# Optimization experiments

Measured on AMD Instinct MI355X. Metric: run time of the kernel, lower is better.

The kernel has to match this reference:

```python
import jax, jax.numpy as jnp
import numpy as np

INPUT_DIM = 2
COUNT_BINS = 16
BOUND = 5.0
FLOW_LENGTH = 4
HIDDEN = 256
MULT = 4 * COUNT_BINS - 1  # 63 param groups per dim (w:K, h:K, d:K-1, lam:K)
MIN_BIN = 1e-3
MIN_DERIV = 1e-3
MIN_LAMBDA = 0.025
N = 131072


def _masks():
    input_idx = np.arange(1, INPUT_DIM + 1)                  # [2]
    hidden_idx = np.arange(HIDDEN) % (INPUT_DIM - 1) + 1     # all ones for input_dim=2
    out_idx = np.tile(input_idx, MULT)                       # [126] -> [1,2,1,2,...]
    m1 = (hidden_idx[:, None] >= input_idx[None, :]).astype(np.float32)   # [H,2]
    m2 = (hidden_idx[:, None] >= hidden_idx[None, :]).astype(np.float32)  # [H,H]
    m3 = (out_idx[:, None] > hidden_idx[None, :]).astype(np.float32)      # [126,H]
    return jnp.asarray(m1), jnp.asarray(m2), jnp.asarray(m3)


def _made(z, W1, b1, W2, b2, W3, b3, m1, m2, m3):
    # masked MLP producing raw spline params, shape [..., MULT, input_dim]
    h = jax.nn.relu(z @ (W1 * m1).T + b1)
    h = jax.nn.relu(h @ (W2 * m2).T + b2)
    out = (h @ (W3 * m3).T + b3).reshape(z.shape[:-1] + (MULT, INPUT_DIM))
    K = COUNT_BINS
    sw = lambda t: jnp.swapaxes(t, -1, -2)  # -> [..., input_dim, K]
    w = sw(out[..., 0:K, :])
    hh = sw(out[..., K:2 * K, :])
    d = sw(out[..., 2 * K:3 * K - 1, :])
    lam = sw(out[..., 3 * K - 1:4 * K - 1, :])
    return w, hh, d, lam


def _spline(x, w_raw, h_raw, d_raw, l_raw):
    # Pyro monotonic linear rational spline (Dolatabadi et al.), forward only.
    K = COUNT_BINS
    left, right = -BOUND, BOUND
    w = jax.nn.softmax(w_raw, axis=-1)
    h = jax.nn.softmax(h_raw, axis=-1)
    d = jax.nn.softplus(d_raw)
    l = jax.nn.sigmoid(l_raw)

    widths = MIN_BIN + (1.0 - MIN_BIN * K) * w
    zpad = jnp.zeros(widths.shape[:-1] + (1,), widths.dtype)
    cw = jnp.concatenate([zpad, jnp.cumsum(widths, -1)], -1)
    cw = (right - left) * cw + left
    cw = cw.at[..., 0].set(left).at[..., -1].set(right)
    widths = cw[..., 1:] - cw[..., :-1]

    heights = MIN_BIN + (1.0 - MIN_BIN * K) * h
    ch = jnp.concatenate([zpad, jnp.cumsum(heights, -1)], -1)
    ch = (right - left) * ch + left
    ch = ch.at[..., 0].set(left).at[..., -1].set(right)
    heights = ch[..., 1:] - ch[..., :-1]

    deriv = MIN_DERIV + d
    onep = jnp.ones(deriv.shape[:-1] + (1,), deriv.dtype)
    deriv = jnp.concatenate([onep, deriv, onep], -1)  # boundary derivs = 1, [.., K+1]

    lam = MIN_LAMBDA + (1.0 - 2.0 * MIN_LAMBDA) * l

    inside = (x >= left) & (x <= right)
    xc = jnp.clip(x, left, right)

    bin_idx = jnp.clip(jnp.sum((xc[..., None] >= cw).astype(jnp.int32), -1) - 1, 0, K - 1)
    ib = bin_idx[..., None]
    g = lambda t: jnp.take_along_axis(t, ib, -1)[..., 0]
    x_k = g(cw)
    w_k = g(widths)
    y_k = g(ch)
    h_k = g(heights)
    d_k = g(deriv)
    d_k1 = jnp.take_along_axis(deriv, ib + 1, -1)[..., 0]
    lam_k = g(lam)

    wa = 1.0
    wb = jnp.sqrt(d_k / d_k1) * wa
    wc = (lam_k * wa * d_k + (1.0 - lam_k) * wb * d_k1) * (w_k / h_k)
    ya = y_k
    yb = h_k + y_k
    yc = ((1.0 - lam_k) * wa * ya + lam_k * wb * yb) / ((1.0 - lam_k) * wa + lam_k * wb)

    theta = (xc - x_k) / w_k
    left_seg = theta <= lam_k
    num = jnp.where(left_seg,
                    wa * ya * (lam_k - theta) + wc * yc * theta,
                    wc * yc * (1.0 - theta) + wb * yb * (theta - lam_k))
    den = jnp.where(left_seg,
                    wa * (lam_k - theta) + wc * theta,
                    wc * (1.0 - theta) + wb * (theta - lam_k))
    y = num / den
    return jnp.where(inside, y, x)  # identity outside [-B, B]


def setup_inputs() -> dict:
    key = jax.random.key(0)
    ks = jax.random.split(key, 7)
    s = 0.05
    return {
        "x": jax.random.normal(ks[0], (N, INPUT_DIM), jnp.float32),
        "W1": jax.random.normal(ks[1], (HIDDEN, INPUT_DIM), jnp.float32) * s,
        "b1": jax.random.normal(ks[2], (HIDDEN,), jnp.float32) * s,
        "W2": jax.random.normal(ks[3], (HIDDEN, HIDDEN), jnp.float32) * s,
        "b2": jax.random.normal(ks[4], (HIDDEN,), jnp.float32) * s,
        "W3": jax.random.normal(ks[5], (MULT * INPUT_DIM, HIDDEN), jnp.float32) * s,
        "b3": jax.random.normal(ks[6], (MULT * INPUT_DIM,), jnp.float32) * s,
    }


def reference(x, W1, b1, W2, b2, W3, b3):
    # forward(): apply the SAME shared spline transform flow_length times,
    # collecting intermediates zs (returned stacked: [L+1, N, 2]).
    m1, m2, m3 = _masks()
    z = x
    zs = [z]
    for _ in range(FLOW_LENGTH):
        w, hh, d, l = _made(z, W1, b1, W2, b2, W3, b3, m1, m2, m3)
        z = _spline(z, w, hh, d, l)
        zs.append(z)
    return jnp.stack(zs)
```

## Files before the change

kernel.cpp:

```cpp
#include <hip/hip_runtime.h>
#include <hip/hip_fp16.h>
#include <math.h>

#define N_SAMPLES 131072
#define HIDDEN    256
#define M_GRID    2048
#define REC       72
#define U_LO      (-8.0f)
#define DELTA     0.0078125f
#define INV_DELTA 128.0f
#define MT3       16
#define STR2      69

__device__ __attribute__((aligned(16))) float g_H2T[M_GRID * HIDDEN];
__device__ __attribute__((aligned(16))) float g_table[M_GRID * REC];
__device__ __attribute__((aligned(16))) float g_knots0[REC];

__device__ __forceinline__ float rcpf(float x) { return __builtin_amdgcn_rcpf(x); }

__device__ __forceinline__ float softplusf(float x) {
  return fmaxf(x, 0.0f) + log1pf(expf(-fabsf(x)));
}

__device__ __forceinline__ unsigned int packh2(float a, float b) {
  __half2 h = __floats2half2_rn(a, b);
  return *(unsigned int*)&h;
}

__device__ __forceinline__ void unpack8(uint4 u, float* f) {
  float2 t;
  t = __half22float2(*(__half2*)&u.x); f[0] = t.x; f[1] = t.y;
  t = __half22float2(*(__half2*)&u.y); f[2] = t.x; f[3] = t.y;
  t = __half22float2(*(__half2*)&u.z); f[4] = t.x; f[5] = t.y;
  t = __half22float2(*(__half2*)&u.w); f[6] = t.x; f[7] = t.y;
}

__device__ void process_column(const float* __restrict__ raw, int stride,
                               float* __restrict__ rec) {
  float v[16];
  float cw[17], ch[17], dv[17], lm[16];
  float mx = -1e30f;
#pragma unroll
  for (int k = 0; k < 16; k++) { v[k] = raw[k * stride]; mx = fmaxf(mx, v[k]); }
  float s = 0.0f;
#pragma unroll
  for (int k = 0; k < 16; k++) { v[k] = expf(v[k] - mx); s += v[k]; }
  float scl = 0.984f / s;
  cw[0] = -5.0f;
  float a = 0.0f;
#pragma unroll
  for (int k = 0; k < 16; k++) {
    a += fmaf(v[k], scl, 0.001f);
    cw[k + 1] = fmaf(a, 10.0f, -5.0f);
  }
  cw[16] = 5.0f;
  mx = -1e30f;
#pragma unroll
  for (int k = 0; k < 16; k++) { v[k] = raw[(16 + k) * stride]; mx = fmaxf(mx, v[k]); }
  s = 0.0f;
#pragma unroll
  for (int k = 0; k < 16; k++) { v[k] = expf(v[k] - mx); s += v[k]; }
  scl = 0.984f / s;
  ch[0] = -5.0f;
  a = 0.0f;
#pragma unroll
  for (int k = 0; k < 16; k++) {
    a += fmaf(v[k], scl, 0.001f);
    ch[k + 1] = fmaf(a, 10.0f, -5.0f);
  }
  ch[16] = 5.0f;
  dv[0] = 1.0f; dv[16] = 1.0f;
#pragma unroll
  for (int j = 0; j < 15; j++) dv[j + 1] = 0.001f + softplusf(raw[(32 + j) * stride]);
#pragma unroll
  for (int k = 0; k < 16; k++) {
    float xx = raw[(47 + k) * stride];
    lm[k] = fmaf(0.95f, 1.0f / (1.0f + expf(-xx)), 0.025f);
  }
  uint4* u4 = (uint4*)rec;
  u4[0] = make_uint4(packh2(cw[0], cw[1]),  packh2(cw[2], cw[3]),
                     packh2(cw[4], cw[5]),  packh2(cw[6], cw[7]));
  u4[1] = make_uint4(packh2(cw[8], cw[9]),  packh2(cw[10], cw[11]),
                     packh2(cw[12], cw[13]), packh2(cw[14], cw[15]));
#pragma unroll
  for (int k = 0; k < 16; k++) {
    u4[2 + k] = make_uint4(packh2(ch[k], ch[k + 1]), packh2(dv[k], dv[k + 1]),
                           packh2(lm[k], cw[k]),     packh2(cw[k + 1], 0.0f));
  }
}

__device__ __forceinline__ float spline_eval(float z, float xk, float xk1,
                                             float yk, float yk1,
                                             float dk, float dk1, float lam) {
  float xc = fminf(fmaxf(z, -5.0f), 5.0f);
  float wk = xk1 - xk;
  float hk = yk1 - yk;
  float wb = __builtin_amdgcn_sqrtf(dk * rcpf(dk1));
  float wc = fmaf(lam, dk, (1.0f - lam) * wb * dk1) * wk * rcpf(hk);
  float ya = yk;
  float yb = yk + hk;
  float yc = fmaf(lam * wb, yb, (1.0f - lam) * ya) * rcpf(fmaf(lam, wb, 1.0f - lam));
  float th = (xc - xk) * rcpf(wk);
  bool left = th <= lam;
  float num = left ? fmaf(ya, lam - th, wc * yc * th)
                   : fmaf(wc * yc, 1.0f - th, wb * yb * (th - lam));
  float den = left ? fmaf(wc, th, lam - th)
                   : fmaf(wc, 1.0f - th, wb * (th - lam));
  float y = num * rcpf(den);
  bool inside = (z >= -5.0f) && (z <= 5.0f);
  return inside ? y : z;
}

__global__ __launch_bounds__(256) void k_gemm2(const float* __restrict__ W1,
                                               const float* __restrict__ b1,
                                               const float* __restrict__ W2,
                                               const float* __restrict__ b2) {
  __shared__ unsigned int sW[128 * STR2];
  __shared__ float2 sAB[256];
  __shared__ float red[3 * 64 * 36];
  const int t = threadIdx.x;
  const int m0 = blockIdx.x * 32;
  const int o0 = blockIdx.y * 64;
  {
    const int ol = t >> 2, seg = t & 3;
    const float* src = W2 + (size_t)(o0 + ol) * 256 + 16 * seg;
#pragma unroll
    for (int c = 0; c < 4; c++) {
#pragma unroll
      for (int q = 0; q < 4; q++) {
        float4 v = *(const float4*)(src + 64 * c + 4 * q);
        const int k2 = (64 * c + 16 * seg + 4 * q) >> 1;
        sW[(k2 + 0) * STR2 + ol] = packh2(v.x, v.y);
        sW[(k2 + 1) * STR2 + ol] = packh2(v.z, v.w);
      }
    }
  }
  sAB[t] = make_float2(W1[2 * t], b1[t]);
  __syncthreads();
  const int w = t >> 6, lane = t & 63;
  const int tp = lane >> 2, tm = lane & 3;
  const float u0 = fmaf((float)(m0 + 8 * tm), DELTA, U_LO);
  float acc[4][8] = {};
  const int kb2 = w * 32;
#pragma unroll 4
  for (int kk = 0; kk < 32; kk++) {
    const int k2 = kb2 + kk;
    uint4 ap = *(const uint4*)&sW[k2 * STR2 + 4 * tp];
    float2 a0 = __half22float2(*(__half2*)&ap.x);
    float2 a1 = __half22float2(*(__half2*)&ap.y);
    float2 a2 = __half22float2(*(__half2*)&ap.z);
    float2 a3 = __half22float2(*(__half2*)&ap.w);
    float2 abe = sAB[2 * k2];
    float2 abo = sAB[2 * k2 + 1];
    float t0e = fmaf(abe.x, u0, abe.y), ste = abe.x * DELTA;
    float t0o = fmaf(abo.x, u0, abo.y), sto = abo.x * DELTA;
    float he[8], ho[8];
#pragma unroll
    for (int j = 0; j < 8; j++) {
      he[j] = fmaxf(fmaf((float)j, ste, t0e), 0.0f);
      ho[j] = fmaxf(fmaf((float)j, sto, t0o), 0.0f);
    }
#pragma unroll
    for (int j = 0; j < 8; j++) {
      acc[0][j] = fmaf(a0.x, he[j], acc[0][j]);
      acc[1][j] = fmaf(a1.x, he[j], acc[1][j]);
      acc[2][j] = fmaf(a2.x, he[j], acc[2][j]);
      acc[3][j] = fmaf(a3.x, he[j], acc[3][j]);
      acc[0][j] = fmaf(a0.y, ho[j], acc[0][j]);
      acc[1][j] = fmaf(a1.y, ho[j], acc[1][j]);
      acc[2][j] = fmaf(a2.y, ho[j], acc[2][j]);
      acc[3][j] = fmaf(a3.y, ho[j], acc[3][j]);
    }
  }
  if (w > 0) {
#pragma unroll
    for (int i = 0; i < 4; i++) {
      *(float4*)&red[((w - 1) * 64 + lane) * 36 + 8 * i] =
          make_float4(acc[i][0], acc[i][1], acc[i][2], acc[i][3]);
      *(float4*)&red[((w - 1) * 64 + lane) * 36 + 8 * i + 4] =
          make_float4(acc[i][4], acc[i][5], acc[i][6], acc[i][7]);
    }
  }
  __syncthreads();
  if (w == 0) {
#pragma unroll
    for (int v = 0; v < 3; v++) {
#pragma unroll
      for (int i = 0; i < 4; i++) {
        float4 r0 = *(const float4*)&red[(v * 64 + lane) * 36 + 8 * i];
        float4 r1 = *(const float4*)&red[(v * 64 + lane) * 36 + 8 * i + 4];
        acc[i][0] += r0.x; acc[i][1] += r0.y; acc[i][2] += r0.z; acc[i][3] += r0.w;
        acc[i][4] += r1.x; acc[i][5] += r1.y; acc[i][6] += r1.z; acc[i][7] += r1.w;
      }
    }
    float4 bb = *(const float4*)&b2[o0 + 4 * tp];
#pragma unroll
    for (int j = 0; j < 8; j++) {
      float4 r;
      r.x = fmaxf(acc[0][j] + bb.x, 0.0f);
      r.y = fmaxf(acc[1][j] + bb.y, 0.0f);
      r.z = fmaxf(acc[2][j] + bb.z, 0.0f);
      r.w = fmaxf(acc[3][j] + bb.w, 0.0f);
      *(float4*)&g_H2T[(size_t)(m0 + 8 * tm + j) * 256 + o0 + 4 * tp] = r;
    }
  }
}

__global__ __launch_bounds__(256) void k_gemm3proc(const float* __restrict__ W3,
                                                   const float* __restrict__ b3) {
  __shared__ unsigned int sW[128 * STR2];
  __shared__ unsigned int sH[128 * 17];
  __shared__ float red[3 * 64 * 20];
  __shared__ float raws[64 * 20];
  const int t = threadIdx.x;
  const int m0 = blockIdx.x * MT3;
  {
    const int ol = t >> 2, seg = t & 3;
    const int row = (ol < 63) ? (2 * ol + 1) : 1;
    const float* src = W3 + (size_t)row * 256 + 16 * seg;
#pragma unroll
    for (int c = 0; c < 4; c++) {
#pragma unroll
      for (int q = 0; q < 4; q++) {
        float4 v = *(const float4*)(src + 64 * c + 4 * q);
        const int k2 = (64 * c + 16 * seg + 4 * q) >> 1;
        sW[(k2 + 0) * STR2 + ol] = packh2(v.x, v.y);
        sW[(k2 + 1) * STR2 + ol] = packh2(v.z, v.w);
      }
    }
  }
  {
    const int j = t & 15, c = t >> 4;
    const float* src = g_H2T + (size_t)(m0 + j) * 256 + 16 * c;
#pragma unroll
    for (int q = 0; q < 4; q++) {
      float4 v = *(const float4*)(src + 4 * q);
      const int k2 = (16 * c + 4 * q) >> 1;
      sH[(k2 + 0) * 17 + j] = packh2(v.x, v.y);
      sH[(k2 + 1) * 17 + j] = packh2(v.z, v.w);
    }
  }
  __syncthreads();
  const int w = t >> 6, lane = t & 63;
  const int tp = lane >> 2, tm = lane & 3;
  float acc[4][4] = {};
  const int kb2 = w * 32;
#pragma unroll 4
  for (int kk = 0; kk < 32; kk++) {
    const int k2 = kb2 + kk;
    uint4 ap = *(const uint4*)&sW[k2 * STR2 + 4 * tp];
    uint4 bp = *(const uint4*)&sH[k2 * 17 + 4 * tm];
    float2 a0 = __half22float2(*(__half2*)&ap.x);
    float2 a1 = __half22float2(*(__half2*)&ap.y);
    float2 a2 = __half22float2(*(__half2*)&ap.z);
    float2 a3 = __half22float2(*(__half2*)&ap.w);
    float2 b0 = __half22float2(*(__half2*)&bp.x);
    float2 b1v = __half22float2(*(__half2*)&bp.y);
    float2 b2v = __half22float2(*(__half2*)&bp.z);
    float2 b3v = __half22float2(*(__half2*)&bp.w);
    float ae[4] = {a0.x, a1.x, a2.x, a3.x};
    float ao[4] = {a0.y, a1.y, a2.y, a3.y};
    float be[4] = {b0.x, b1v.x, b2v.x, b3v.x};
    float bo[4] = {b0.y, b1v.y, b2v.y, b3v.y};
#pragma unroll
    for (int i = 0; i < 4; i++) {
#pragma unroll
      for (int j = 0; j < 4; j++) {
        acc[i][j] = fmaf(ae[i], be[j], acc[i][j]);
        acc[i][j] = fmaf(ao[i], bo[j], acc[i][j]);
      }
    }
  }
  if (w > 0) {
#pragma unroll
    for (int i = 0; i < 4; i++)
      *(float4*)&red[((w - 1) * 64 + lane) * 20 + 4 * i] =
          make_float4(acc[i][0], acc[i][1], acc[i][2], acc[i][3]);
  }
  __syncthreads();
  if (w == 0) {
#pragma unroll
    for (int v = 0; v < 3; v++) {
#pragma unroll
      for (int i = 0; i < 4; i++) {
        float4 r = *(const float4*)&red[(v * 64 + lane) * 20 + 4 * i];
        acc[i][0] += r.x; acc[i][1] += r.y; acc[i][2] += r.z; acc[i][3] += r.w;
      }
    }
#pragma unroll
    for (int i = 0; i < 4; i++) {
      const int p = 4 * tp + i;
      const int bi = (p < 63) ? (2 * p + 1) : 1;
      const float bias = b3[bi];
      *(float4*)&raws[p * 20 + 4 * tm] =
          make_float4(acc[i][0] + bias, acc[i][1] + bias,
                      acc[i][2] + bias, acc[i][3] + bias);
    }
  }
  __syncthreads();
  if (t < MT3) process_column(&raws[t], 20, g_table + (size_t)(m0 + t) * REC);
  if (t == 64 && blockIdx.x == 0) process_column(b3, 2, g_knots0);
}

__global__ __launch_bounds__(256) void k_main(const float* __restrict__ x,
                                              float* __restrict__ out) {
  __shared__ __attribute__((aligned(16))) float kn0[REC];
  for (int j = threadIdx.x; j < REC; j += 256) kn0[j] = g_knots0[j];
  __syncthreads();
  float kf0[16];
  {
    uint4 q0 = *(const uint4*)(kn0);
    uint4 q1 = *(const uint4*)(kn0 + 4);
    unpack8(q0, kf0);
    unpack8(q1, kf0 + 8);
  }
  const int i = blockIdx.x * 256 + threadIdx.x;
  const float2 xv = ((const float2*)x)[i];
  float z0 = xv.x, z1 = xv.y;
  ((float2*)out)[i] = xv;
  for (int t = 0; t < 4; t++) {
    float tt = (z0 - U_LO) * INV_DELTA;
    int i0 = (int)floorf(tt);
    i0 = min(max(i0, 0), M_GRID - 2);
    float f = fminf(fmaxf(tt - (float)i0, 0.0f), 1.0f);
    const float* r0 = g_table + (size_t)i0 * REC;
    float kf[16];
    {
      uint4 q0 = *(const uint4*)(r0);
      uint4 q1 = *(const uint4*)(r0 + 4);
      unpack8(q0, kf);
      unpack8(q1, kf + 8);
    }
    float xc1 = fminf(fmaxf(z1, -5.0f), 5.0f);
    int k1 = 0;
#pragma unroll
    for (int j = 1; j < 16; j++) k1 += (xc1 >= kf[j]) ? 1 : 0;
    const float* c0 = r0 + 8 + 4 * k1;
    uint4 A = *(const uint4*)c0;
    uint4 B = *(const uint4*)(c0 + REC);
    float2 Ay = __half22float2(*(__half2*)&A.x);
    float2 Ad = __half22float2(*(__half2*)&A.y);
    float2 Al = __half22float2(*(__half2*)&A.z);
    float2 Ax = __half22float2(*(__half2*)&A.w);
    float2 By = __half22float2(*(__half2*)&B.x);
    float2 Bd = __half22float2(*(__half2*)&B.y);
    float2 Bl = __half22float2(*(__half2*)&B.z);
    float2 Bx = __half22float2(*(__half2*)&B.w);
    float yk  = fmaf(f, By.x - Ay.x, Ay.x);
    float yk1 = fmaf(f, By.y - Ay.y, Ay.y);
    float dk  = fmaf(f, Bd.x - Ad.x, Ad.x);
    float dk1 = fmaf(f, Bd.y - Ad.y, Ad.y);
    float lam = fmaf(f, Bl.x - Al.x, Al.x);
    float xk  = fmaf(f, Bl.y - Al.y, Al.y);
    float xk1 = fmaf(f, Bx.x - Ax.x, Ax.x);
    float z1n = spline_eval(z1, xk, xk1, yk, yk1, dk, dk1, lam);
    float xc0 = fminf(fmaxf(z0, -5.0f), 5.0f);
    int k0 = 0;
#pragma unroll
    for (int j = 1; j < 16; j++) k0 += (xc0 >= kf0[j]) ? 1 : 0;
    uint4 C = *(const uint4*)&kn0[8 + 4 * k0];
    float2 Cy = __half22float2(*(__half2*)&C.x);
    float2 Cd = __half22float2(*(__half2*)&C.y);
    float2 Cl = __half22float2(*(__half2*)&C.z);
    float2 Cx = __half22float2(*(__half2*)&C.w);
    float z0n = spline_eval(z0, Cl.y, Cx.x, Cy.x, Cy.y, Cd.x, Cd.y, Cl.x);
    z0 = z0n; z1 = z1n;
    ((float2*)(out + (size_t)(t + 1) * (N_SAMPLES * 2)))[i] = make_float2(z0, z1);
  }
}

extern "C" void kernel_launch(void* const* d_in, const int* in_sizes, int n_in,
                              void* d_out, int out_size, void* d_ws, size_t ws_size,
                              hipStream_t stream) {
  const float* x  = (const float*)d_in[0];
  const float* W1 = (const float*)d_in[1];
  const float* b1 = (const float*)d_in[2];
  const float* W2 = (const float*)d_in[3];
  const float* b2 = (const float*)d_in[4];
  const float* W3 = (const float*)d_in[5];
  const float* b3 = (const float*)d_in[6];
  float* out = (float*)d_out;
  hipLaunchKernelGGL(k_gemm2, dim3(M_GRID / 32, 4), dim3(256), 0, stream, W1, b1, W2, b2);
  hipLaunchKernelGGL(k_gemm3proc, dim3(M_GRID / MT3), dim3(256), 0, stream, W3, b3);
  hipLaunchKernelGGL(k_main, dim3(N_SAMPLES / 256), dim3(256), 0, stream, x, out);
}
```

Before: 103.1 us.

## Parallelize spline table construction across 16 lanes and halve GEMM3 row tile

The per-column spline parameter processing, previously done serially by one thread per grid point, is now spread over 16 lanes. Softmax max and sum use xor shuffles, cumulative knots use a shuffle scan, and neighbouring knots come from shuffle-up. The GEMM3 tile per block drops from 16 to 8 grid rows, which doubles the block count and shrinks shared memory and accumulators per thread. The aim is to remove the long serial tail where only 16 threads per block did all the exp and softplus work. In exchange each block reloads W3 into shared memory again, so total redundant W3 traffic doubles.

```diff
diff --git a/kernel.cpp b/kernel.cpp
--- a/kernel.cpp
+++ b/kernel.cpp
@@ -9,7 +9,7 @@
 #define U_LO      (-8.0f)
 #define DELTA     0.0078125f
 #define INV_DELTA 128.0f
-#define MT3       16
+#define MT3       8
 #define STR2      69
 
 __device__ __attribute__((aligned(16))) float g_H2T[M_GRID * HIDDEN];
@@ -35,58 +35,53 @@
   t = __half22float2(*(__half2*)&u.w); f[6] = t.x; f[7] = t.y;
 }
 
-__device__ void process_column(const float* __restrict__ raw, int stride,
-                               float* __restrict__ rec) {
-  float v[16];
-  float cw[17], ch[17], dv[17], lm[16];
-  float mx = -1e30f;
-#pragma unroll
-  for (int k = 0; k < 16; k++) { v[k] = raw[k * stride]; mx = fmaxf(mx, v[k]); }
-  float s = 0.0f;
-#pragma unroll
-  for (int k = 0; k < 16; k++) { v[k] = expf(v[k] - mx); s += v[k]; }
-  float scl = 0.984f / s;
-  cw[0] = -5.0f;
-  float a = 0.0f;
-#pragma unroll
-  for (int k = 0; k < 16; k++) {
-    a += fmaf(v[k], scl, 0.001f);
-    cw[k + 1] = fmaf(a, 10.0f, -5.0f);
-  }
-  cw[16] = 5.0f;
-  mx = -1e30f;
-#pragma unroll
-  for (int k = 0; k < 16; k++) { v[k] = raw[(16 + k) * stride]; mx = fmaxf(mx, v[k]); }
-  s = 0.0f;
-#pragma unroll
-  for (int k = 0; k < 16; k++) { v[k] = expf(v[k] - mx); s += v[k]; }
-  scl = 0.984f / s;
-  ch[0] = -5.0f;
-  a = 0.0f;
-#pragma unroll
-  for (int k = 0; k < 16; k++) {
-    a += fmaf(v[k], scl, 0.001f);
-    ch[k + 1] = fmaf(a, 10.0f, -5.0f);
-  }
-  ch[16] = 5.0f;
-  dv[0] = 1.0f; dv[16] = 1.0f;
-#pragma unroll
-  for (int j = 0; j < 15; j++) dv[j + 1] = 0.001f + softplusf(raw[(32 + j) * stride]);
-#pragma unroll
-  for (int k = 0; k < 16; k++) {
-    float xx = raw[(47 + k) * stride];
-    lm[k] = fmaf(0.95f, 1.0f / (1.0f + expf(-xx)), 0.025f);
-  }
-  uint4* u4 = (uint4*)rec;
-  u4[0] = make_uint4(packh2(cw[0], cw[1]),  packh2(cw[2], cw[3]),
-                     packh2(cw[4], cw[5]),  packh2(cw[6], cw[7]));
-  u4[1] = make_uint4(packh2(cw[8], cw[9]),  packh2(cw[10], cw[11]),
-                     packh2(cw[12], cw[13]), packh2(cw[14], cw[15]));
-#pragma unroll
-  for (int k = 0; k < 16; k++) {
-    u4[2 + k] = make_uint4(packh2(ch[k], ch[k + 1]), packh2(dv[k], dv[k + 1]),
-                           packh2(lm[k], cw[k]),     packh2(cw[k + 1], 0.0f));
-  }
+__device__ __forceinline__ void process16(float wv, float hv, float dvr,
+                                          float lamv, int kl,
+                                          float* __restrict__ rec) {
+  float mx = wv;
+#pragma unroll
+  for (int d = 1; d < 16; d <<= 1) mx = fmaxf(mx, __shfl_xor(mx, d, 16));
+  float v = expf(wv - mx);
+  float s = v;
+#pragma unroll
+  for (int d = 1; d < 16; d <<= 1) s += __shfl_xor(s, d, 16);
+  float inc = fmaf(v, 0.984f * rcpf(s), 0.001f);
+  float cum = inc;
+#pragma unroll
+  for (int d = 1; d < 16; d <<= 1) {
+    float n = __shfl_up(cum, d, 16);
+    if (kl >= d) cum += n;
+  }
+  float cwk1 = (kl == 15) ? 5.0f : fmaf(cum, 10.0f, -5.0f);
+  float cwk = __shfl_up(cwk1, 1, 16);
+  if (kl == 0) cwk = -5.0f;
+  float mh = hv;
+#pragma unroll
+  for (int d = 1; d < 16; d <<= 1) mh = fmaxf(mh, __shfl_xor(mh, d, 16));
+  float vh = expf(hv - mh);
+  float sh = vh;
+#pragma unroll
+  for (int d = 1; d < 16; d <<= 1) sh += __shfl_xor(sh, d, 16);
+  float inch = fmaf(vh, 0.984f * rcpf(sh), 0.001f);
+  float cumh = inch;
+#pragma unroll
+  for (int d = 1; d < 16; d <<= 1) {
+    float n = __shfl_up(cumh, d, 16);
+    if (kl >= d) cumh += n;
+  }
+  float chk1 = (kl == 15) ? 5.0f : fmaf(cumh, 10.0f, -5.0f);
+  float chk = __shfl_up(chk1, 1, 16);
+  if (kl == 0) chk = -5.0f;
+  float dvk1 = (kl < 15) ? (0.001f + softplusf(dvr)) : 1.0f;
+  float dvk = __shfl_up(dvk1, 1, 16);
+  if (kl == 0) dvk = 1.0f;
+  float lm = fmaf(0.95f, 1.0f / (1.0f + expf(-lamv)), 0.025f);
+  uint4 ck = make_uint4(packh2(chk, chk1), packh2(dvk, dvk1),
+                        packh2(lm, cwk), packh2(cwk1, 0.0f));
+  ((uint4*)rec)[2 + kl] = ck;
+  float cA = __shfl(cwk, 2 * kl, 16);
+  float cB = __shfl(cwk, 2 * kl + 1, 16);
+  if (kl < 8) ((unsigned int*)rec)[kl] = packh2(cA, cB);
 }
 
 __device__ __forceinline__ float spline_eval(float z, float xk, float xk1,
@@ -209,9 +204,9 @@
 __global__ __launch_bounds__(256) void k_gemm3proc(const float* __restrict__ W3,
                                                    const float* __restrict__ b3) {
   __shared__ unsigned int sW[128 * STR2];
-  __shared__ unsigned int sH[128 * 17];
-  __shared__ float red[3 * 64 * 20];
-  __shared__ float raws[64 * 20];
+  __shared__ unsigned int sH[128 * 9];
+  __shared__ float red[3 * 64 * 8];
+  __shared__ float raws[64 * 9];
   const int t = threadIdx.x;
   const int m0 = blockIdx.x * MT3;
   {
@@ -230,52 +225,48 @@
     }
   }
   {
-    const int j = t & 15, c = t >> 4;
-    const float* src = g_H2T + (size_t)(m0 + j) * 256 + 16 * c;
-#pragma unroll
-    for (int q = 0; q < 4; q++) {
-      float4 v = *(const float4*)(src + 4 * q);
-      const int k2 = (16 * c + 4 * q) >> 1;
-      sH[(k2 + 0) * 17 + j] = packh2(v.x, v.y);
-      sH[(k2 + 1) * 17 + j] = packh2(v.z, v.w);
-    }
+    const int j = t & 7, c = t >> 3;
+    const float* src = g_H2T + (size_t)(m0 + j) * 256 + 8 * c;
+    float4 f0 = *(const float4*)(src);
+    float4 f1 = *(const float4*)(src + 4);
+    sH[(4 * c + 0) * 9 + j] = packh2(f0.x, f0.y);
+    sH[(4 * c + 1) * 9 + j] = packh2(f0.z, f0.w);
+    sH[(4 * c + 2) * 9 + j] = packh2(f1.x, f1.y);
+    sH[(4 * c + 3) * 9 + j] = packh2(f1.z, f1.w);
   }
   __syncthreads();
   const int w = t >> 6, lane = t & 63;
   const int tp = lane >> 2, tm = lane & 3;
-  float acc[4][4] = {};
+  float acc[4][2] = {};
   const int kb2 = w * 32;
 #pragma unroll 4
   for (int kk = 0; kk < 32; kk++) {
     const int k2 = kb2 + kk;
     uint4 ap = *(const uint4*)&sW[k2 * STR2 + 4 * tp];
-    uint4 bp = *(const uint4*)&sH[k2 * 17 + 4 * tm];
+    uint2 bp = *(const uint2*)&sH[k2 * 9 + 2 * tm];
     float2 a0 = __half22float2(*(__half2*)&ap.x);
     float2 a1 = __half22float2(*(__half2*)&ap.y);
     float2 a2 = __half22float2(*(__half2*)&ap.z);
     float2 a3 = __half22float2(*(__half2*)&ap.w);
     float2 b0 = __half22float2(*(__half2*)&bp.x);
     float2 b1v = __half22float2(*(__half2*)&bp.y);
-    float2 b2v = __half22float2(*(__half2*)&bp.z);
-    float2 b3v = __half22float2(*(__half2*)&bp.w);
     float ae[4] = {a0.x, a1.x, a2.x, a3.x};
     float ao[4] = {a0.y, a1.y, a2.y, a3.y};
-    float be[4] = {b0.x, b1v.x, b2v.x, b3v.x};
-    float bo[4] = {b0.y, b1v.y, b2v.y, b3v.y};
 #pragma unroll
     for (int i = 0; i < 4; i++) {
-#pragma unroll
-      for (int j = 0; j < 4; j++) {
-        acc[i][j] = fmaf(ae[i], be[j], acc[i][j]);
-        acc[i][j] = fmaf(ao[i], bo[j], acc[i][j]);
-      }
-    }
-  }
+      acc[i][0] = fmaf(ae[i], b0.x, acc[i][0]);
+      acc[i][0] = fmaf(ao[i], b0.y, acc[i][0]);
+      acc[i][1] = fmaf(ae[i], b1v.x, acc[i][1]);
+      acc[i][1] = fmaf(ao[i], b1v.y, acc[i][1]);
+    }
+  }
+  __syncthreads();
   if (w > 0) {
 #pragma unroll
-    for (int i = 0; i < 4; i++)
-      *(float4*)&red[((w - 1) * 64 + lane) * 20 + 4 * i] =
-          make_float4(acc[i][0], acc[i][1], acc[i][2], acc[i][3]);
+    for (int i = 0; i < 4; i++) {
+      red[((w - 1) * 64 + lane) * 8 + 2 * i + 0] = acc[i][0];
+      red[((w - 1) * 64 + lane) * 8 + 2 * i + 1] = acc[i][1];
+    }
   }
   __syncthreads();
   if (w == 0) {
@@ -283,8 +274,8 @@
     for (int v = 0; v < 3; v++) {
 #pragma unroll
       for (int i = 0; i < 4; i++) {
-        float4 r = *(const float4*)&red[(v * 64 + lane) * 20 + 4 * i];
-        acc[i][0] += r.x; acc[i][1] += r.y; acc[i][2] += r.z; acc[i][3] += r.w;
+        acc[i][0] += red[(v * 64 + lane) * 8 + 2 * i + 0];
+        acc[i][1] += red[(v * 64 + lane) * 8 + 2 * i + 1];
       }
     }
 #pragma unroll
@@ -292,14 +283,26 @@
       const int p = 4 * tp + i;
       const int bi = (p < 63) ? (2 * p + 1) : 1;
       const float bias = b3[bi];
-      *(float4*)&raws[p * 20 + 4 * tm] =
-          make_float4(acc[i][0] + bias, acc[i][1] + bias,
-                      acc[i][2] + bias, acc[i][3] + bias);
-    }
-  }
-  __syncthreads();
-  if (t < MT3) process_column(&raws[t], 20, g_table + (size_t)(m0 + t) * REC);
-  if (t == 64 && blockIdx.x == 0) process_column(b3, 2, g_knots0);
+      raws[p * 9 + 2 * tm + 0] = acc[i][0] + bias;
+      raws[p * 9 + 2 * tm + 1] = acc[i][1] + bias;
+    }
+  }
+  __syncthreads();
+  if (t < 128) {
+    const int c = t >> 4, kl = t & 15;
+    float wv = raws[kl * 9 + c];
+    float hv = raws[(16 + kl) * 9 + c];
+    float dvr = raws[(32 + kl) * 9 + c];
+    float lamv = raws[(47 + kl) * 9 + c];
+    process16(wv, hv, dvr, lamv, kl, g_table + (size_t)(m0 + c) * REC);
+  } else if (blockIdx.x == 0 && (t >> 4) == 8) {
+    const int kl = t & 15;
+    float wv = b3[2 * kl];
+    float hv = b3[2 * (16 + kl)];
+    float dvr = b3[2 * (32 + kl)];
+    float lamv = b3[2 * (47 + kl)];
+    process16(wv, hv, dvr, lamv, kl, g_knots0);
+  }
 }
 
 __global__ __launch_bounds__(256) void k_main(const float* __restrict__ x,
```

Result: faster. 90.00 us (-12.7%).
